# Kernel tuning notes

Measured on AMD Instinct MI355X. Metric: run time of the kernel, lower is better.

## Reference

```python
import math
import jax, jax.numpy as jnp
import numpy as np

NUM_HEAD = 16
BLOCK_SIZE = 2048

def get_slopes(n):
    def pow2(n):
        start = 2 ** (-2 ** (-(math.log2(n) - 3)))
        return [start * start ** i for i in range(n)]
    if math.log2(n).is_integer():
        return pow2(n)
    c = 2 ** math.floor(math.log2(n))
    return pow2(c) + get_slopes(2 * c)[0::2][: n - c]

def setup_inputs() -> dict:
    key = jax.random.key(0)
    ks = jax.random.split(key, 5)
    B, T, C = 4, 2048, 1024
    x = jax.random.normal(ks[0], (B, T, C), dtype=jnp.float32)
    Wq = 0.02 * jax.random.normal(ks[1], (C, C), dtype=jnp.float32)
    Wk = 0.02 * jax.random.normal(ks[2], (C, C), dtype=jnp.float32)
    Wv = 0.02 * jax.random.normal(ks[3], (C, C), dtype=jnp.float32)
    Wo = 0.02 * jax.random.normal(ks[4], (C, C), dtype=jnp.float32)
    return {"x": x, "Wq": Wq, "Wk": Wk, "Wv": Wv, "Wo": Wo}

def reference(x, Wq, Wk, Wv, Wo):
    B, T, C = x.shape
    nh, hd = NUM_HEAD, C // NUM_HEAD
    # projections, split heads -> [B, nh, T, hd]
    q = (x @ Wq).reshape(B, T, nh, hd).transpose(0, 2, 1, 3)
    k = (x @ Wk).reshape(B, T, nh, hd).transpose(0, 2, 1, 3)
    v = (x @ Wv).reshape(B, T, nh, hd).transpose(0, 2, 1, 3)
    # full [B, nh, T, T] scores (module materializes these)
    attn = jnp.einsum("bhqd,bhkd->bhqk", q, k) / jnp.sqrt(jnp.float32(hd))
    # ALiBi bias as in create_mask: slope * (j - (block_size - 1)), key-position only
    slopes = jnp.asarray(get_slopes(nh), dtype=jnp.float32)  # [nh]
    bias = slopes[:, None] * (jnp.arange(T, dtype=jnp.float32) - (BLOCK_SIZE - 1))  # [nh, T]
    attn = attn + bias[None, :, None, :]
    # causal mask + stable softmax in fp32
    causal = jnp.tril(jnp.ones((T, T), dtype=bool))
    masked = jnp.where(causal[None, None], attn.astype(jnp.float32), jnp.finfo(jnp.float32).min)
    probs = jax.nn.softmax(masked, axis=-1)
    out = jnp.einsum("bhqk,bhkd->bhqd", probs, v)  # [B, nh, T, hd]
    out = out.transpose(0, 2, 1, 3).reshape(B, T, C)
    return out @ Wo
```

## Files before the change

### kernel.cpp

```cpp
#include <hip/hip_runtime.h>
#include <hip/hip_bf16.h>

#define TSEQ   2048
#define CDIM   1024
#define NHEAD  16
#define HDIM   64

typedef float f32x4  __attribute__((ext_vector_type(4)));
typedef float f32x16v __attribute__((ext_vector_type(16)));
typedef __bf16 bf16x8 __attribute__((ext_vector_type(8)));
typedef unsigned short u16x8 __attribute__((ext_vector_type(8)));
typedef unsigned short u16x4 __attribute__((ext_vector_type(4)));
typedef unsigned int   u32x4 __attribute__((ext_vector_type(4)));

#define QSCALE 0.18033688011112042f
#define LOG2E  1.4426950408889634f

static __device__ __forceinline__ unsigned short f2bf(float f) {
    unsigned u = __builtin_bit_cast(unsigned, f);
    unsigned r = u + 0x7FFFu + ((u >> 16) & 1u);
    return (unsigned short)(r >> 16);
}

static __device__ __forceinline__ f32x4 mfma16(u16x8 a, u16x8 b, f32x4 c) {
    return __builtin_amdgcn_mfma_f32_16x16x32_bf16(
        __builtin_bit_cast(bf16x8, a), __builtin_bit_cast(bf16x8, b), c, 0, 0, 0);
}
static __device__ __forceinline__ f32x16v mfma32(u16x8 a, u16x8 b, f32x16v c) {
    return __builtin_amdgcn_mfma_f32_32x32x16_bf16(
        __builtin_bit_cast(bf16x8, a), __builtin_bit_cast(bf16x8, b), c, 0, 0, 0);
}

static __device__ __forceinline__ void gload16(const void* g, void* l) {
    __builtin_amdgcn_global_load_lds(
        (const __attribute__((address_space(1))) unsigned int*)g,
        (__attribute__((address_space(3))) unsigned int*)l, 16, 0, 0);
}


__global__ __launch_bounds__(256) void castx(
    const float* __restrict__ x, unsigned short* __restrict__ xb)
{
    int t = blockIdx.x * 256 + threadIdx.x;
    f32x4 v = *(const f32x4*)&x[t * 4];
    u16x4 o;
    o[0] = f2bf(v[0]); o[1] = f2bf(v[1]); o[2] = f2bf(v[2]); o[3] = f2bf(v[3]);
    *(u16x4*)&xb[t * 4] = o;
}

__global__ __launch_bounds__(256) void wtcast(
    const float* __restrict__ wq, const float* __restrict__ wk,
    const float* __restrict__ wv, const float* __restrict__ wo,
    unsigned short* __restrict__ wt)
{
    __shared__ unsigned short t[64 * 72];
    const int z = blockIdx.z;
    const float* src = (z == 0) ? wq : (z == 1) ? wk : (z == 2) ? wv : wo;
    const int k0 = blockIdx.x * 64, n0 = blockIdx.y * 64, tid = threadIdx.x;

    #pragma unroll
    for (int i = 0; i < 4; ++i) {
        int idx = i * 256 + tid;
        int r = idx >> 4, c4 = idx & 15;
        f32x4 v = *(const f32x4*)&src[(k0 + r) * 1024 + n0 + c4 * 4];
        u16x4 o;
        o[0] = f2bf(v[0]); o[1] = f2bf(v[1]); o[2] = f2bf(v[2]); o[3] = f2bf(v[3]);
        *(u16x4*)&t[r * 72 + c4 * 4] = o;
    }
    __syncthreads();
    #pragma unroll
    for (int i = 0; i < 2; ++i) {
        int idx = i * 256 + tid;
        int n = idx >> 3, k8 = idx & 7;
        u16x8 o;
        #pragma unroll
        for (int e = 0; e < 8; ++e) o[e] = t[(k8 * 8 + e) * 72 + n];
        *(u16x8*)&wt[z * 1048576 + (n0 + n) * 1024 + k0 + k8 * 8] = o;
    }
}

template<int MODE>
__global__ __launch_bounds__(256) void gemm_gl(
    const unsigned short* __restrict__ A, const unsigned short* __restrict__ WT,
    unsigned short* __restrict__ outb, float* __restrict__ outf)
{
    __shared__ __align__(16) unsigned short Al[128 * 64];
    __shared__ __align__(16) unsigned short Bl[128 * 64];

    const int tid  = threadIdx.x;
    const int z    = blockIdx.z;
    const int m0   = blockIdx.y * 128;
    const int n0   = blockIdx.x * 128;
    const unsigned short* W = WT + (MODE == 0 ? z * 1048576 : 0);

    const int wid  = tid >> 6, lane = tid & 63;
    const int wr   = (wid >> 1) * 64, wc = (wid & 1) * 64;
    const int lrow = lane & 15, lk = (lane >> 4) * 8;

    f32x4 acc[4][4] = {};

    for (int kt = 0; kt < 16; ++kt) {
        __syncthreads();
        #pragma unroll
        for (int c = 0; c < 4; ++c) {
            int cz = wid * 4 + c;
            int row = cz * 8 + (lane >> 3), col = (lane & 7) * 8;
            gload16(&A[(m0 + row) * 1024 + kt * 64 + col], &Al[cz * 512]);
            gload16(&W[(n0 + row) * 1024 + kt * 64 + col], &Bl[cz * 512]);
        }
        __syncthreads();
        #pragma unroll
        for (int ks = 0; ks < 2; ++ks) {
            u16x8 af[4], bfr[4];
            #pragma unroll
            for (int m = 0; m < 4; ++m)
                af[m] = *(const u16x8*)&Al[(wr + m * 16 + lrow) * 64 + ks * 32 + lk];
            #pragma unroll
            for (int n = 0; n < 4; ++n)
                bfr[n] = *(const u16x8*)&Bl[(wc + n * 16 + lrow) * 64 + ks * 32 + lk];
            #pragma unroll
            for (int m = 0; m < 4; ++m)
                #pragma unroll
                for (int n = 0; n < 4; ++n)
                    acc[m][n] = mfma16(af[m], bfr[n], acc[m][n]);
        }
    }

    const int g = lane >> 4;
    #pragma unroll
    for (int m = 0; m < 4; ++m)
        #pragma unroll
        for (int n = 0; n < 4; ++n)
            #pragma unroll
            for (int j = 0; j < 4; ++j) {
                int grow = m0 + wr + m * 16 + g * 4 + j;
                int gcol = n0 + wc + n * 16 + lrow;
                float val = acc[m][n][j];
                if (MODE == 0) {
                    int b = grow >> 11, t = grow & 2047;
                    int h = gcol >> 6,  d = gcol & 63;
                    if (z == 0) val *= QSCALE;
                    if (z == 2)
                        outb[z * 8388608 + (((b << 4) + h) * 64 + d) * 2048 + t] = f2bf(val);
                    else
                        outb[z * 8388608 + (((b << 4) + h) * 2048 + t) * 64 + d] = f2bf(val);
                } else {
                    outf[grow * 1024 + gcol] = val;
                }
            }
}

__global__ __launch_bounds__(512, 2) void attn8s(
    const unsigned short* __restrict__ qh, const unsigned short* __restrict__ kh,
    const unsigned short* __restrict__ vt, unsigned short* __restrict__ aout)
{
    __shared__ __align__(16) unsigned short Kl[2][128 * 64];
    __shared__ __align__(16) unsigned short Vl[2][64 * 128];

    const int bh  = blockIdx.y;
    const int h   = bh & 15, b = bh >> 4;
    const int c   = (bh < 32) ? (7 - (int)blockIdx.x) : (int)blockIdx.x;
    const int tid = threadIdx.x, wid = tid >> 6, lane = tid & 63;
    const int l31 = lane & 31, hi = lane >> 5;

    const unsigned short* Qb = qh + bh * (TSEQ * HDIM);
    const unsigned short* Kb = kh + bh * (TSEQ * HDIM);
    const unsigned short* Vb = vt + bh * (TSEQ * HDIM);

    const float slope2 = exp2f(-0.5f * (float)(h + 1)) * LOG2E;
    const int   Wwin   = (int)ceilf(40.0f / slope2);

    int blo = c * 256 - Wwin;
    const int t0     = (blo > 0) ? (blo >> 7) : 0;
    const int t_last = 2 * c + 1;

    const int qw = c * 256 + wid * 32;
    const int qg = qw + l31;

    const int krow = lane >> 3;
    const int kgc  = (lane & 7) ^ krow;
    const int vrow = lane >> 4;
    const int vcc  = lane & 15;

#define STAGE(BUF, KV) do {                                                   \
    _Pragma("unroll")                                                         \
    for (int i_ = 0; i_ < 2; ++i_) {                                          \
        int cz_ = wid * 2 + i_;                                    \
        gload16(&Kb[((KV) + cz_ * 8 + krow) * 64 + kgc * 8],                  \
                &Kl[BUF][cz_ * 512]);                                         \
        int d_ = cz_ * 4 + vrow;                                              \
        int gc_ = vcc ^ (d_ & 15);                                            \
        gload16(&Vb[d_ * 2048 + (KV) + gc_ * 8], &Vl[BUF][cz_ * 512]);        \
    } } while (0)

    u16x8 qf[4];
    #pragma unroll
    for (int kf = 0; kf < 4; ++kf)
        qf[kf] = *(const u16x8*)&Qb[qg * 64 + kf * 16 + hi * 8];
    float m_r = -1e30f, l_r = 0.f;
    f32x16v Ot[2] = {};

    STAGE(0, t0 * 128);
    int cur = 0;

    for (int t = t0; t <= t_last; ++t) {
        const int kv0 = t * 128;
        __syncthreads();

        if (t < t_last) STAGE(cur ^ 1, (t + 1) * 128);

        if (kv0 <= qw + 31 && kv0 + 127 >= qw - Wwin) {
            const int v0 = qw - kv0;
            int nkv2 = (v0 >> 5) + 1; if (nkv2 > 4) nkv2 = 4;
            const bool diag = (kv0 + 127 > qw);

            f32x16v st[4];
            __builtin_amdgcn_s_setprio(1);
            #pragma unroll
            for (int kv2 = 0; kv2 < 4; ++kv2) {
                if (kv2 < nkv2) {
                    f32x16v a = {};
                    #pragma unroll
                    for (int kf = 0; kf < 4; ++kf) {
                        u16x8 ka = *(const u16x8*)&Kl[cur][(kv2 * 32 + l31) * 64 +
                                                           (((kf * 2 + hi) ^ (l31 & 7)) * 8)];
                        a = mfma32(ka, qf[kf], a);
                    }
                    st[kv2] = a;
                } else {
                    st[kv2] = (f32x16v)(-1e30f);
                }
            }
            __builtin_amdgcn_s_setprio(0);

            if (diag) {
                #pragma unroll
                for (int kv2 = 0; kv2 < 4; ++kv2) {
                    if (kv2 < nkv2) {
                        #pragma unroll
                        for (int r = 0; r < 16; ++r) {
                            int kv = kv0 + kv2 * 32 + (r & 3) + 8 * (r >> 2) + 4 * hi;
                            if (kv > qg) st[kv2][r] = -1e30f;
                        }
                    }
                }
            }

            float t16[16];
            #pragma unroll
            for (int i = 0; i < 16; ++i)
                t16[i] = fmaxf(fmaxf(st[0][i], st[1][i]), fmaxf(st[2][i], st[3][i]));
            #pragma unroll
            for (int i = 0; i < 8; ++i) t16[i] = fmaxf(t16[i], t16[i + 8]);
            #pragma unroll
            for (int i = 0; i < 4; ++i) t16[i] = fmaxf(t16[i], t16[i + 4]);
            float rm = fmaxf(fmaxf(t16[0], t16[1]), fmaxf(t16[2], t16[3]));
            rm = fmaxf(rm, __shfl_xor(rm, 32, 64));

            int kvmax = kv0 + 127; if (kvmax > qw + 31) kvmax = qw + 31;
            float cand = rm + slope2 * (float)(kvmax - 2047);

            if (!__all(cand - m_r <= 8.0f)) {
                float mn = fmaxf(m_r, cand);
                float alpha = exp2f(m_r - mn);
                m_r = mn;
                l_r *= alpha;
                Ot[0] *= alpha;
                Ot[1] *= alpha;
            }

            unsigned pku[4][8];
            float s16[16] = {};
            #pragma unroll
            for (int kv2 = 0; kv2 < 4; ++kv2) {
                if (kv2 < nkv2) {
                    float base2 = slope2 * (float)(kv0 + kv2 * 32 + 4 * hi - 2047) - m_r;
                    #pragma unroll
                    for (int r = 0; r < 16; ++r) {
                        float koff = (float)((r & 3) + 8 * (r >> 2));
                        st[kv2][r] = exp2f(st[kv2][r] + fmaf(slope2, koff, base2));
                        s16[r] += st[kv2][r];
                    }
                    #pragma unroll
                    for (int idx = 0; idx < 8; ++idx) {
                        unsigned lo2 = __builtin_bit_cast(unsigned short, (__bf16)st[kv2][2 * idx]);
                        unsigned hh = __builtin_bit_cast(unsigned short, (__bf16)st[kv2][2 * idx + 1]);
                        pku[kv2][idx] = lo2 | (hh << 16);
                    }
                }
            }
            #pragma unroll
            for (int i = 0; i < 8; ++i) s16[i] += s16[i + 8];
            #pragma unroll
            for (int i = 0; i < 4; ++i) s16[i] += s16[i + 4];
            float rs = (s16[0] + s16[1]) + (s16[2] + s16[3]);
            rs += __shfl_xor(rs, 32, 64);
            l_r += rs;

            __builtin_amdgcn_s_setprio(1);
            #pragma unroll
            for (int kf = 0; kf < 8; ++kf) {
                if ((kf >> 1) < nkv2) {
                    const int kv2 = kf >> 1, base = 4 * (kf & 1);
                    unsigned s0 = hi ? pku[kv2][base + 0] : pku[kv2][base + 2];
                    unsigned s1 = hi ? pku[kv2][base + 1] : pku[kv2][base + 3];
                    unsigned r0 = __shfl_xor(s0, 32, 64);
                    unsigned r1 = __shfl_xor(s1, 32, 64);
                    u32x4 w;
                    w[0] = hi ? r0 : pku[kv2][base + 0];
                    w[1] = hi ? r1 : pku[kv2][base + 1];
                    w[2] = hi ? pku[kv2][base + 2] : r0;
                    w[3] = hi ? pku[kv2][base + 3] : r1;
                    u16x8 pb = __builtin_bit_cast(u16x8, w);
                    #pragma unroll
                    for (int dn = 0; dn < 2; ++dn) {
                        u16x8 va = *(const u16x8*)&Vl[cur][(dn * 32 + l31) * 128 +
                                                           (((kf * 2 + hi) ^ (l31 & 15)) * 8)];
                        Ot[dn] = mfma32(va, pb, Ot[dn]);
                    }
                }
            }
            __builtin_amdgcn_s_setprio(0);
        }

        cur ^= 1;
    }

    float rl = 1.0f / l_r;
    #pragma unroll
    for (int dn = 0; dn < 2; ++dn)
        #pragma unroll
        for (int rq = 0; rq < 4; ++rq) {
            u16x4 o;
            #pragma unroll
            for (int jj = 0; jj < 4; ++jj)
                o[jj] = f2bf(Ot[dn][rq * 4 + jj] * rl);
            int d = dn * 32 + 8 * rq + 4 * hi;
            *(u16x4*)&aout[(b * 2048 + qg) * 1024 + h * 64 + d] = o;
        }
#undef STAGE
}

extern "C" void kernel_launch(void* const* d_in, const int* in_sizes, int n_in,
                              void* d_out, int out_size, void* d_ws, size_t ws_size,
                              hipStream_t stream)
{
    const float* x  = (const float*)d_in[0];
    const float* Wq = (const float*)d_in[1];
    const float* Wk = (const float*)d_in[2];
    const float* Wv = (const float*)d_in[3];
    const float* Wo = (const float*)d_in[4];

    unsigned short* ws = (unsigned short*)d_ws;
    unsigned short* wb = ws;
    unsigned short* xb = ws + 4194304;
    unsigned short* qh = ws + 12582912;
    unsigned short* kh = qh + 8388608;
    unsigned short* vt = kh + 8388608;
    unsigned short* ao = xb;

    castx<<<dim3(8192), dim3(256), 0, stream>>>(x, xb);
    wtcast<<<dim3(16, 16, 4), dim3(256), 0, stream>>>(Wq, Wk, Wv, Wo, wb);
    gemm_gl<0><<<dim3(8, 64, 3), dim3(256), 0, stream>>>(xb, wb, qh, (float*)nullptr);
    attn8s<<<dim3(8, 64), dim3(512), 0, stream>>>(qh, kh, vt, ao);
    gemm_gl<1><<<dim3(8, 64, 1), dim3(256), 0, stream>>>(
        ao, wb + 3 * 1048576, (unsigned short*)nullptr, (float*)d_out);
}
```

Baseline: 227.4 us.

## Split heavy causal attention chunks across two blocks and merge with combine kernel

Each pair of attention blocks now handles one heavy query chunk (7-j) and one light chunk (j). The heavy chunk's KV range is split at tile 9: segment 0 takes the first part and writes an unnormalized bf16 partial plus running max and sum to workspace. Segment 1 takes the remainder and then processes the light chunk in full. A new combine2 kernel rescales and merges the two partials for chunks 4..7. The aim is to balance per-block work, since later causal chunks with wide ALiBi windows dominate the tail. The cost is an extra launch, extra global traffic for the partials, and extra bf16 rounding of the unnormalized partial outputs.

```diff
diff --git a/kernel.cpp b/kernel.cpp
--- a/kernel.cpp
+++ b/kernel.cpp
@@ -20,6 +20,10 @@
     unsigned u = __builtin_bit_cast(unsigned, f);
     unsigned r = u + 0x7FFFu + ((u >> 16) & 1u);
     return (unsigned short)(r >> 16);
+}
+static __device__ __forceinline__ float bf2f(unsigned short u) {
+    unsigned v = ((unsigned)u) << 16;
+    return __builtin_bit_cast(float, v);
 }
 
 static __device__ __forceinline__ f32x4 mfma16(u16x8 a, u16x8 b, f32x4 c) {
@@ -150,16 +154,19 @@
             }
 }
 
-__global__ __launch_bounds__(512, 2) void attn8s(
+__global__ __launch_bounds__(512, 2) void attnsp(
     const unsigned short* __restrict__ qh, const unsigned short* __restrict__ kh,
-    const unsigned short* __restrict__ vt, unsigned short* __restrict__ aout)
+    const unsigned short* __restrict__ vt, unsigned short* __restrict__ part,
+    float* __restrict__ mlb, unsigned short* __restrict__ aout)
 {
     __shared__ __align__(16) unsigned short Kl[2][128 * 64];
     __shared__ __align__(16) unsigned short Vl[2][64 * 128];
 
+    const int j   = blockIdx.x >> 1, seg = blockIdx.x & 1;
     const int bh  = blockIdx.y;
     const int h   = bh & 15, b = bh >> 4;
-    const int c   = (bh < 32) ? (7 - (int)blockIdx.x) : (int)blockIdx.x;
+    const int cA  = 7 - j, cB = j;
+    const int slot = bh * 4 + (cA - 4);
     const int tid = threadIdx.x, wid = tid >> 6, lane = tid & 63;
     const int l31 = lane & 31, hi = lane >> 5;
 
@@ -170,12 +177,9 @@
     const float slope2 = exp2f(-0.5f * (float)(h + 1)) * LOG2E;
     const int   Wwin   = (int)ceilf(40.0f / slope2);
 
-    int blo = c * 256 - Wwin;
-    const int t0     = (blo > 0) ? (blo >> 7) : 0;
-    const int t_last = 2 * c + 1;
-
-    const int qw = c * 256 + wid * 32;
-    const int qg = qw + l31;
+    int a0 = cA * 256 - Wwin; const int t0A = (a0 > 0) ? (a0 >> 7) : 0;
+    int b0 = cB * 256 - Wwin; const int t0B = (b0 > 0) ? (b0 >> 7) : 0;
+    const int nphase = seg ? 2 : 1;
 
     const int krow = lane >> 3;
     const int kgc  = (lane & 7) ^ krow;
@@ -193,152 +197,229 @@
         gload16(&Vb[d_ * 2048 + (KV) + gc_ * 8], &Vl[BUF][cz_ * 512]);        \
     } } while (0)
 
-    u16x8 qf[4];
-    #pragma unroll
-    for (int kf = 0; kf < 4; ++kf)
-        qf[kf] = *(const u16x8*)&Qb[qg * 64 + kf * 16 + hi * 8];
-    float m_r = -1e30f, l_r = 0.f;
-    f32x16v Ot[2] = {};
-
-    STAGE(0, t0 * 128);
-    int cur = 0;
-
-    for (int t = t0; t <= t_last; ++t) {
-        const int kv0 = t * 128;
+    for (int ph = 0; ph < nphase; ++ph) {
+        const int c   = ph ? cB : cA;
+        const int tlo = ph ? t0B : (seg ? ((t0A > 9) ? t0A : 9) : t0A);
+        const int thi = ph ? (2 * cB + 1) : (seg ? (2 * cA + 1) : 8);
+
+        const int qw = c * 256 + wid * 32;
+        const int qg = qw + l31;
+        u16x8 qf[4];
+        #pragma unroll
+        for (int kf = 0; kf < 4; ++kf)
+            qf[kf] = *(const u16x8*)&Qb[qg * 64 + kf * 16 + hi * 8];
+        float m_r = -1e30f, l_r = 0.f;
+        f32x16v Ot[2] = {};
+
         __syncthreads();
-
-        if (t < t_last) STAGE(cur ^ 1, (t + 1) * 128);
-
-        if (kv0 <= qw + 31 && kv0 + 127 >= qw - Wwin) {
-            const int v0 = qw - kv0;
-            int nkv2 = (v0 >> 5) + 1; if (nkv2 > 4) nkv2 = 4;
-            const bool diag = (kv0 + 127 > qw);
-
-            f32x16v st[4];
-            __builtin_amdgcn_s_setprio(1);
-            #pragma unroll
-            for (int kv2 = 0; kv2 < 4; ++kv2) {
-                if (kv2 < nkv2) {
-                    f32x16v a = {};
-                    #pragma unroll
-                    for (int kf = 0; kf < 4; ++kf) {
-                        u16x8 ka = *(const u16x8*)&Kl[cur][(kv2 * 32 + l31) * 64 +
-                                                           (((kf * 2 + hi) ^ (l31 & 7)) * 8)];
-                        a = mfma32(ka, qf[kf], a);
-                    }
-                    st[kv2] = a;
-                } else {
-                    st[kv2] = (f32x16v)(-1e30f);
-                }
-            }
-            __builtin_amdgcn_s_setprio(0);
-
-            if (diag) {
-                #pragma unroll
-                for (int kv2 = 0; kv2 < 4; ++kv2) {
-                    if (kv2 < nkv2) {
-                        #pragma unroll
-                        for (int r = 0; r < 16; ++r) {
-                            int kv = kv0 + kv2 * 32 + (r & 3) + 8 * (r >> 2) + 4 * hi;
-                            if (kv > qg) st[kv2][r] = -1e30f;
+        if (tlo <= thi) {
+            STAGE(0, tlo * 128);
+            int cur = 0;
+            for (int t = tlo; t <= thi; ++t) {
+                const int kv0 = t * 128;
+                __syncthreads();
+
+                if (t < thi) STAGE(cur ^ 1, (t + 1) * 128);
+
+                if (kv0 <= qw + 31 && kv0 + 127 >= qw - Wwin) {
+                    const int v0 = qw - kv0;
+                    int nkv2 = (v0 >> 5) + 1;
+                    if (nkv2 > 4) nkv2 = 4;
+                    if (nkv2 < 1) nkv2 = 1;
+                    const bool diag = (kv0 + 127 > qw);
+
+                    f32x16v st[4];
+                    __builtin_amdgcn_s_setprio(1);
+                    #pragma unroll
+                    for (int kv2 = 0; kv2 < 4; ++kv2) {
+                        if (kv2 < nkv2) {
+                            f32x16v a = {};
+                            #pragma unroll
+                            for (int kf = 0; kf < 4; ++kf) {
+                                u16x8 ka = *(const u16x8*)&Kl[cur][(kv2 * 32 + l31) * 64 +
+                                                                   (((kf * 2 + hi) ^ (l31 & 7)) * 8)];
+                                a = mfma32(ka, qf[kf], a);
+                            }
+                            st[kv2] = a;
+                        } else {
+                            st[kv2] = (f32x16v)(-1e30f);
                         }
                     }
+                    __builtin_amdgcn_s_setprio(0);
+
+                    if (diag) {
+                        #pragma unroll
+                        for (int kv2 = 0; kv2 < 4; ++kv2) {
+                            if (kv2 < nkv2) {
+                                #pragma unroll
+                                for (int r = 0; r < 16; ++r) {
+                                    int kv = kv0 + kv2 * 32 + (r & 3) + 8 * (r >> 2) + 4 * hi;
+                                    if (kv > qg) st[kv2][r] = -1e30f;
+                                }
+                            }
+                        }
+                    }
+
+                    float t16[16];
+                    #pragma unroll
+                    for (int i = 0; i < 16; ++i)
+                        t16[i] = fmaxf(fmaxf(st[0][i], st[1][i]), fmaxf(st[2][i], st[3][i]));
+                    #pragma unroll
+                    for (int i = 0; i < 8; ++i) t16[i] = fmaxf(t16[i], t16[i + 8]);
+                    #pragma unroll
+                    for (int i = 0; i < 4; ++i) t16[i] = fmaxf(t16[i], t16[i + 4]);
+                    float rm = fmaxf(fmaxf(t16[0], t16[1]), fmaxf(t16[2], t16[3]));
+                    rm = fmaxf(rm, __shfl_xor(rm, 32, 64));
+
+                    int kvmax = kv0 + 127; if (kvmax > qw + 31) kvmax = qw + 31;
+                    float cand = rm + slope2 * (float)(kvmax - 2047);
+
+                    if (!__all(cand - m_r <= 8.0f)) {
+                        float mn = fmaxf(m_r, cand);
+                        float alpha = exp2f(m_r - mn);
+                        m_r = mn;
+                        l_r *= alpha;
+                        Ot[0] *= alpha;
+                        Ot[1] *= alpha;
+                    }
+
+                    unsigned pku[4][8];
+                    float s16[16] = {};
+                    #pragma unroll
+                    for (int kv2 = 0; kv2 < 4; ++kv2) {
+                        if (kv2 < nkv2) {
+                            float base2 = slope2 * (float)(kv0 + kv2 * 32 + 4 * hi - 2047) - m_r;
+                            #pragma unroll
+                            for (int r = 0; r < 16; ++r) {
+                                float koff = (float)((r & 3) + 8 * (r >> 2));
+                                st[kv2][r] = exp2f(st[kv2][r] + fmaf(slope2, koff, base2));
+                                s16[r] += st[kv2][r];
+                            }
+                            #pragma unroll
+                            for (int idx = 0; idx < 8; ++idx) {
+                                unsigned lo2 = __builtin_bit_cast(unsigned short, (__bf16)st[kv2][2 * idx]);
+                                unsigned hh = __builtin_bit_cast(unsigned short, (__bf16)st[kv2][2 * idx + 1]);
+                                pku[kv2][idx] = lo2 | (hh << 16);
+                            }
+                        }
+                    }
+                    #pragma unroll
+                    for (int i = 0; i < 8; ++i) s16[i] += s16[i + 8];
+                    #pragma unroll
+                    for (int i = 0; i < 4; ++i) s16[i] += s16[i + 4];
+                    float rs = (s16[0] + s16[1]) + (s16[2] + s16[3]);
+                    rs += __shfl_xor(rs, 32, 64);
+                    l_r += rs;
+
+                    __builtin_amdgcn_s_setprio(1);
+                    #pragma unroll
+                    for (int kf = 0; kf < 8; ++kf) {
+                        if ((kf >> 1) < nkv2) {
+                            const int kv2 = kf >> 1, base = 4 * (kf & 1);
+                            unsigned s0 = hi ? pku[kv2][base + 0] : pku[kv2][base + 2];
+                            unsigned s1 = hi ? pku[kv2][base + 1] : pku[kv2][base + 3];
+                            unsigned r0 = __shfl_xor(s0, 32, 64);
+                            unsigned r1 = __shfl_xor(s1, 32, 64);
+                            u32x4 w;
+                            w[0] = hi ? r0 : pku[kv2][base + 0];
+                            w[1] = hi ? r1 : pku[kv2][base + 1];
+                            w[2] = hi ? pku[kv2][base + 2] : r0;
+                            w[3] = hi ? pku[kv2][base + 3] : r1;
+                            u16x8 pb = __builtin_bit_cast(u16x8, w);
+                            #pragma unroll
+                            for (int dn = 0; dn < 2; ++dn) {
+                                u16x8 va = *(const u16x8*)&Vl[cur][(dn * 32 + l31) * 128 +
+                                                                   (((kf * 2 + hi) ^ (l31 & 15)) * 8)];
+                                Ot[dn] = mfma32(va, pb, Ot[dn]);
+                            }
+                        }
+                    }
+                    __builtin_amdgcn_s_setprio(0);
                 }
+
+                cur ^= 1;
             }
-
-            float t16[16];
-            #pragma unroll
-            for (int i = 0; i < 16; ++i)
-                t16[i] = fmaxf(fmaxf(st[0][i], st[1][i]), fmaxf(st[2][i], st[3][i]));
-            #pragma unroll
-            for (int i = 0; i < 8; ++i) t16[i] = fmaxf(t16[i], t16[i + 8]);
-            #pragma unroll
-            for (int i = 0; i < 4; ++i) t16[i] = fmaxf(t16[i], t16[i + 4]);
-            float rm = fmaxf(fmaxf(t16[0], t16[1]), fmaxf(t16[2], t16[3]));
-            rm = fmaxf(rm, __shfl_xor(rm, 32, 64));
-
-            int kvmax = kv0 + 127; if (kvmax > qw + 31) kvmax = qw + 31;
-            float cand = rm + slope2 * (float)(kvmax - 2047);
-
-            if (!__all(cand - m_r <= 8.0f)) {
-                float mn = fmaxf(m_r, cand);
-                float alpha = exp2f(m_r - mn);
-                m_r = mn;
-                l_r *= alpha;
-                Ot[0] *= alpha;
-                Ot[1] *= alpha;
-            }
-
-            unsigned pku[4][8];
-            float s16[16] = {};
-            #pragma unroll
-            for (int kv2 = 0; kv2 < 4; ++kv2) {
-                if (kv2 < nkv2) {
-                    float base2 = slope2 * (float)(kv0 + kv2 * 32 + 4 * hi - 2047) - m_r;
-                    #pragma unroll
-                    for (int r = 0; r < 16; ++r) {
-                        float koff = (float)((r & 3) + 8 * (r >> 2));
-                        st[kv2][r] = exp2f(st[kv2][r] + fmaf(slope2, koff, base2));
-                        s16[r] += st[kv2][r];
-                    }
-                    #pragma unroll
-                    for (int idx = 0; idx < 8; ++idx) {
-                        unsigned lo2 = __builtin_bit_cast(unsigned short, (__bf16)st[kv2][2 * idx]);
-                        unsigned hh = __builtin_bit_cast(unsigned short, (__bf16)st[kv2][2 * idx + 1]);
-                        pku[kv2][idx] = lo2 | (hh << 16);
-                    }
+        }
+
+        const int qloc = wid * 32 + l31;
+        if (ph == 0 && seg == 0) {
+            unsigned short* P = part + slot * 16384;
+            #pragma unroll
+            for (int dn = 0; dn < 2; ++dn)
+                #pragma unroll
+                for (int rq = 0; rq < 4; ++rq) {
+                    u16x4 o;
+                    #pragma unroll
+                    for (int jj = 0; jj < 4; ++jj)
+                        o[jj] = f2bf(Ot[dn][rq * 4 + jj]);
+                    int d = dn * 32 + 8 * rq + 4 * hi;
+                    *(u16x4*)&P[qloc * 64 + d] = o;
                 }
-            }
-            #pragma unroll
-            for (int i = 0; i < 8; ++i) s16[i] += s16[i + 8];
-            #pragma unroll
-            for (int i = 0; i < 4; ++i) s16[i] += s16[i + 4];
-            float rs = (s16[0] + s16[1]) + (s16[2] + s16[3]);
-            rs += __shfl_xor(rs, 32, 64);
-            l_r += rs;
-
-            __builtin_amdgcn_s_setprio(1);
-            #pragma unroll
-            for (int kf = 0; kf < 8; ++kf) {
-                if ((kf >> 1) < nkv2) {
-                    const int kv2 = kf >> 1, base = 4 * (kf & 1);
-                    unsigned s0 = hi ? pku[kv2][base + 0] : pku[kv2][base + 2];
-                    unsigned s1 = hi ? pku[kv2][base + 1] : pku[kv2][base + 3];
-                    unsigned r0 = __shfl_xor(s0, 32, 64);
-                    unsigned r1 = __shfl_xor(s1, 32, 64);
-                    u32x4 w;
-                    w[0] = hi ? r0 : pku[kv2][base + 0];
-                    w[1] = hi ? r1 : pku[kv2][base + 1];
-                    w[2] = hi ? pku[kv2][base + 2] : r0;
-                    w[3] = hi ? pku[kv2][base + 3] : r1;
-                    u16x8 pb = __builtin_bit_cast(u16x8, w);
-                    #pragma unroll
-                    for (int dn = 0; dn < 2; ++dn) {
-                        u16x8 va = *(const u16x8*)&Vl[cur][(dn * 32 + l31) * 128 +
-                                                           (((kf * 2 + hi) ^ (l31 & 15)) * 8)];
-                        Ot[dn] = mfma32(va, pb, Ot[dn]);
-                    }
+            mlb[(slot * 2 + 0) * 512 + qloc * 2 + 0] = m_r;
+            mlb[(slot * 2 + 0) * 512 + qloc * 2 + 1] = l_r;
+        } else if (ph == 0) {
+            #pragma unroll
+            for (int dn = 0; dn < 2; ++dn)
+                #pragma unroll
+                for (int rq = 0; rq < 4; ++rq) {
+                    u16x4 o;
+                    #pragma unroll
+                    for (int jj = 0; jj < 4; ++jj)
+                        o[jj] = f2bf(Ot[dn][rq * 4 + jj]);
+                    int d = dn * 32 + 8 * rq + 4 * hi;
+                    *(u16x4*)&aout[(b * 2048 + qg) * 1024 + h * 64 + d] = o;
                 }
-            }
-            __builtin_amdgcn_s_setprio(0);
+            mlb[(slot * 2 + 1) * 512 + qloc * 2 + 0] = m_r;
+            mlb[(slot * 2 + 1) * 512 + qloc * 2 + 1] = l_r;
+        } else {
+            float rl = 1.0f / l_r;
+            #pragma unroll
+            for (int dn = 0; dn < 2; ++dn)
+                #pragma unroll
+                for (int rq = 0; rq < 4; ++rq) {
+                    u16x4 o;
+                    #pragma unroll
+                    for (int jj = 0; jj < 4; ++jj)
+                        o[jj] = f2bf(Ot[dn][rq * 4 + jj] * rl);
+                    int d = dn * 32 + 8 * rq + 4 * hi;
+                    *(u16x4*)&aout[(b * 2048 + qg) * 1024 + h * 64 + d] = o;
+                }
         }
-
-        cur ^= 1;
     }
-
-    float rl = 1.0f / l_r;
+#undef STAGE
+}
+
+__global__ __launch_bounds__(256) void combine2(
+    const unsigned short* __restrict__ part, const float* __restrict__ mlb,
+    unsigned short* __restrict__ aout)
+{
+    const int cx = blockIdx.x;
+    const int bh = blockIdx.y;
+    const int h  = bh & 15, b = bh >> 4;
+    const int slot = bh * 4 + cx;
+    const int q  = threadIdx.x;
+
+    float m0 = mlb[(slot * 2 + 0) * 512 + q * 2 + 0];
+    float l0 = mlb[(slot * 2 + 0) * 512 + q * 2 + 1];
+    float m1 = mlb[(slot * 2 + 1) * 512 + q * 2 + 0];
+    float l1 = mlb[(slot * 2 + 1) * 512 + q * 2 + 1];
+    float M  = fmaxf(m0, m1);
+    float w0 = exp2f(m0 - M), w1 = exp2f(m1 - M);
+    float rl = 1.0f / (l0 * w0 + l1 * w1);
+
+    const unsigned short* P0 = part + slot * 16384 + q * 64;
+    unsigned short* dst = aout + ((b * 2048 + (4 + cx) * 256 + q) * 1024 + h * 64);
+
     #pragma unroll
-    for (int dn = 0; dn < 2; ++dn)
-        #pragma unroll
-        for (int rq = 0; rq < 4; ++rq) {
-            u16x4 o;
-            #pragma unroll
-            for (int jj = 0; jj < 4; ++jj)
-                o[jj] = f2bf(Ot[dn][rq * 4 + jj] * rl);
-            int d = dn * 32 + 8 * rq + 4 * hi;
-            *(u16x4*)&aout[(b * 2048 + qg) * 1024 + h * 64 + d] = o;
-        }
-#undef STAGE
+    for (int i = 0; i < 8; ++i) {
+        u16x8 a0 = *(const u16x8*)&P0[i * 8];
+        u16x8 a1 = *(const u16x8*)&dst[i * 8];
+        u16x8 o;
+        #pragma unroll
+        for (int e = 0; e < 8; ++e)
+            o[e] = f2bf((bf2f(a0[e]) * w0 + bf2f(a1[e]) * w1) * rl);
+        *(u16x8*)&dst[i * 8] = o;
+    }
 }
 
 extern "C" void kernel_launch(void* const* d_in, const int* in_sizes, int n_in,
@@ -357,12 +438,15 @@
     unsigned short* qh = ws + 12582912;
     unsigned short* kh = qh + 8388608;
     unsigned short* vt = kh + 8388608;
+    unsigned short* part = ws + 37748736;
+    float* mlb = (float*)(ws + 41943040);
     unsigned short* ao = xb;
 
     castx<<<dim3(8192), dim3(256), 0, stream>>>(x, xb);
     wtcast<<<dim3(16, 16, 4), dim3(256), 0, stream>>>(Wq, Wk, Wv, Wo, wb);
     gemm_gl<0><<<dim3(8, 64, 3), dim3(256), 0, stream>>>(xb, wb, qh, (float*)nullptr);
-    attn8s<<<dim3(8, 64), dim3(512), 0, stream>>>(qh, kh, vt, ao);
+    attnsp<<<dim3(8, 64), dim3(512), 0, stream>>>(qh, kh, vt, part, mlb, ao);
+    combine2<<<dim3(4, 64), dim3(256), 0, stream>>>(part, mlb, ao);
     gemm_gl<1><<<dim3(8, 64, 1), dim3(256), 0, stream>>>(
         ao, wb + 3 * 1048576, (unsigned short*)nullptr, (float*)d_out);
 }
```

Result: slower. 237.0 us (+4.2%).
